# Kernel optimization log

Hardware: AMD Instinct MI355X
Metric: run time of the kernel (lower is better)

The kernel has to match this reference:

```python
import jax, jax.numpy as jnp
import numpy as np

B, L = 2048, 64          # batch, seq_len (title length)
H, DK = 20, 20           # heads, per-head dim (d_k = d_v = 20)
V, D = 50000, 300        # vocab, word embedding dim
HD = H * DK              # 400


def setup_inputs() -> dict:
    key = jax.random.key(0)
    ks = jax.random.split(key, 12)
    n = lambda k, shape, sc: jax.random.normal(k, shape, dtype=jnp.float32) * sc
    return {
        "text": jax.random.randint(ks[0], (B, L), 0, V),
        "emb": n(ks[1], (V, D), 0.1),
        "WQ": n(ks[2], (D, HD), 0.05), "bQ": jnp.zeros((HD,), jnp.float32),
        "WK": n(ks[3], (D, HD), 0.05), "bK": jnp.zeros((HD,), jnp.float32),
        "WV": n(ks[4], (D, HD), 0.05), "bV": jnp.zeros((HD,), jnp.float32),
        "W1": n(ks[5], (HD, 200), 0.05), "b1": jnp.zeros((200,), jnp.float32),
        "W2": n(ks[6], (200, 1), 0.05), "b2": jnp.zeros((1,), jnp.float32),
    }


def reference(text, emb, WQ, bQ, WK, bK, WV, bV, W1, b1, W2, b2):
    # Embedding lookup (dropout is identity at eval)
    x = emb[text]                                            # [B, L, D]
    b, l = x.shape[0], x.shape[1]

    # Multi-head self-attention with unstable exp-softmax (faithful to source)
    q = (x @ WQ + bQ).reshape(b, l, H, DK)                   # [B, L, H, DK]
    k = (x @ WK + bK).reshape(b, l, H, DK)
    v = (x @ WV + bV).reshape(b, l, H, DK)
    scores = jnp.einsum("bqhd,bkhd->bhqk", q, k) / np.float32(np.sqrt(DK))
    scores = jnp.exp(scores)                                 # [B, H, L, L]
    attn = scores / (jnp.sum(scores, axis=-1, keepdims=True) + 1e-8)
    ctx = jnp.einsum("bhqk,bkhd->bqhd", attn, v).reshape(b, l, HD)  # [B, L, 400]

    # Additive attention pooling (linear -> tanh -> linear -> exp-normalize -> weighted sum)
    e = jnp.tanh(ctx @ W1 + b1)                              # [B, L, 200]
    alpha = jnp.exp(e @ W2 + b2)                             # [B, L, 1]
    alpha = alpha / (jnp.sum(alpha, axis=1, keepdims=True) + 1e-8)
    return jnp.sum(ctx * alpha, axis=1)                      # [B, 400]
```

## Files before the change

kernel.cpp:

```cpp
#include <hip/hip_runtime.h>
#include <hip/hip_bf16.h>

#define B_   2048
#define L_   64
#define H_   20
#define DK_  20
#define D_   300
#define HD_  400
#define F1_  200

typedef __attribute__((ext_vector_type(8))) short short8;
typedef __attribute__((ext_vector_type(4))) float f32x4;

#define WQKV_TILES   800
#define W1_TILES     169
#define W1_OFF_U16   409600
#define CTX_OFF_B    1048576
#define CTX_BYTES    (2048L * 64 * 400 * 2)
#define WS_FULL      (CTX_OFF_B + CTX_BYTES)

__device__ __forceinline__ float b2f(unsigned short u) {
    union { unsigned int i; float f; } v; v.i = ((unsigned int)u) << 16; return v.f;
}
__device__ __forceinline__ unsigned int f2b2(float a, float b) {
    union { __hip_bfloat162 h; unsigned int u; } cv;
    cv.h = __float22bfloat162_rn(make_float2(a, b));
    return cv.u;
}
__device__ __forceinline__ unsigned short f2b(float a) {
    union { __hip_bfloat16 h; unsigned short u; } cv;
    cv.h = __float2bfloat16(a);
    return cv.u;
}
__device__ __forceinline__ float rcpf(float x) { return __builtin_amdgcn_rcpf(x); }
__device__ __forceinline__ float rlane(float v, int l) {
    return __int_as_float(__builtin_amdgcn_readlane(__float_as_int(v), l));
}

__global__ void pack_weights_new(const float* __restrict__ WQ, const float* __restrict__ WK,
                                 const float* __restrict__ WV, const float* __restrict__ W1,
                                 unsigned short* __restrict__ wsp)
{
    const int tid  = blockIdx.x * 256 + threadIdx.x;
    const int frag = tid >> 6, l = tid & 63;
    if (frag >= WQKV_TILES + W1_TILES) return;
    const int octet = l >> 4, lo = l & 15;
    unsigned short v[8];
    if (frag < WQKV_TILES) {
        const int hg = frag / 80, r = frag % 80, kt = r / 8, nt = r % 8;
        const int nl = nt * 16 + lo;
        const int sel = (nl < 120) ? nl / 40 : 0;
        const int within = nl % 40;
        const int h2 = within / 20, d = within % 20;
        const int col = (hg * 2 + h2) * 20 + d;
        const float* W = (sel == 0) ? WQ : (sel == 1) ? WK : WV;
        #pragma unroll
        for (int j = 0; j < 8; ++j) {
            const int k = kt * 32 + octet * 8 + j;
            const float f = (nl < 120 && k < 300) ? W[k * 400 + col] : 0.f;
            v[j] = f2b(f);
        }
    } else {
        const int f2 = frag - WQKV_TILES, kt = f2 / 13, nt = f2 % 13;
        const int n = nt * 16 + lo;
        #pragma unroll
        for (int j = 0; j < 8; ++j) {
            const int k = kt * 32 + octet * 8 + j;
            const float f = (n < 200 && k < 400) ? W1[k * 200 + n] : 0.f;
            v[j] = f2b(f);
        }
    }
    unsigned short* dst = wsp + (long)frag * 512 + l * 8;
    *(ushort4*)(dst)     = make_ushort4(v[0], v[1], v[2], v[3]);
    *(ushort4*)(dst + 4) = make_ushort4(v[4], v[5], v[6], v[7]);
}

template<int S>
__device__ __forceinline__ void a_step(int hg0, int w, int l, bool act, int selbase,
                                       const unsigned short* xp,
                                       const unsigned short* __restrict__ wsp,
                                       const float* bq, f32x4 slab[][4])
{
    #pragma unroll
    for (int s = 0; s < S; ++s) {
        const float bv = act ? bq[selbase + (hg0 + s) * 40] : 0.f;
        #pragma unroll
        for (int mt = 0; mt < 4; ++mt) slab[s][mt] = (f32x4){bv, bv, bv, bv};
    }
    for (int kt = 0; kt < 10; ++kt) {
        short8 a[4];
        #pragma unroll
        for (int mt = 0; mt < 4; ++mt)
            a[mt] = *(const short8*)(xp + ((mt * 10 + kt) * 64 + l) * 8);
        #pragma unroll
        for (int s = 0; s < S; ++s) {
            const short8 bf = *(const short8*)(wsp + ((long)((hg0 + s) * 80 + kt * 8 + w) * 512) + l * 8);
            #pragma unroll
            for (int mt = 0; mt < 4; ++mt)
                slab[s][mt] = __builtin_amdgcn_mfma_f32_16x16x32_bf16(a[mt], bf, slab[s][mt], 0, 0, 0);
        }
    }
}

__device__ __forceinline__ void attn_hg_body(
    int hg, const f32x4* sl, int b, int t, int l, int w,
    bool act, int sel, int baseQK, int baseV, int quad,
    unsigned short* trans, unsigned short* vBs, unsigned short* stage,
    float* rsum_s, unsigned short* __restrict__ ctx_ws)
{
    if (hg > 0) {
        for (int u = t; u < 640; u += 512) {
            const int row = u / 10, c4 = u - row * 10;
            const ushort4 v = *(const ushort4*)(stage + row * 40 + c4 * 4);
            *(ushort4*)(ctx_ws + ((long)(b * 64 + row)) * 400 + (hg - 1) * 40 + c4 * 4) = v;
        }
    }
    if (act) {
        const unsigned int u01a = f2b2(sl[0][0], sl[0][1]), u23a = f2b2(sl[0][2], sl[0][3]);
        const unsigned int u01b = f2b2(sl[1][0], sl[1][1]), u23b = f2b2(sl[1][2], sl[1][3]);
        const unsigned int u01c = f2b2(sl[2][0], sl[2][1]), u23c = f2b2(sl[2][2], sl[2][3]);
        const unsigned int u01d = f2b2(sl[3][0], sl[3][1]), u23d = f2b2(sl[3][2], sl[3][3]);
        const unsigned int p01[4] = {u01a, u01b, u01c, u01d};
        const unsigned int p23[4] = {u23a, u23b, u23c, u23d};
        if (sel < 2) {
            #pragma unroll
            for (int mt = 0; mt < 4; ++mt) {
                const int a0 = baseQK + mt * 512;
                trans[a0]      = (unsigned short)p01[mt];
                trans[a0 + 8]  = (unsigned short)(p01[mt] >> 16);
                trans[a0 + 16] = (unsigned short)p23[mt];
                trans[a0 + 24] = (unsigned short)(p23[mt] >> 16);
            }
        } else {
            #pragma unroll
            for (int mt = 0; mt < 4; ++mt) {
                const int bm = baseV + (mt >> 1) * 1024 + (mt & 1) * 256;
                #pragma unroll
                for (int ii = 0; ii < 4; ++ii) {
                    const int tq = quad * 4 + ii;
                    const unsigned int uu = (ii < 2) ? p01[mt] : p23[mt];
                    vBs[bm + (tq >> 3) * 128 + (tq & 7)] =
                        (unsigned short)((ii & 1) ? (uu >> 16) : uu);
                }
            }
        }
    }
    __syncthreads();

    const int h = w >> 2, jt = w & 3;
    f32x4 accS[4];
    #pragma unroll
    for (int mt = 0; mt < 4; ++mt) accS[mt] = (f32x4){0.f, 0.f, 0.f, 0.f};
    {
        short8 qa[4];
        #pragma unroll
        for (int mt = 0; mt < 4; ++mt)
            qa[mt] = *(const short8*)(trans + ((h * 4 + mt) * 64 + l) * 8);
        const short8 kb = *(const short8*)(trans + 4096 + ((h * 4 + jt) * 64 + l) * 8);
        #pragma unroll
        for (int mt = 0; mt < 4; ++mt)
            accS[mt] = __builtin_amdgcn_mfma_f32_16x16x32_bf16(qa[mt], kb, accS[mt], 0, 0, 0);
    }
    __syncthreads();
    {
        const int jtok = jt * 16 + (l & 15);
        const int ktp = jtok >> 5;
        #pragma unroll
        for (int mt = 0; mt < 4; ++mt) {
            const float e0 = __expf(accS[mt][0] * 0.22360679774997896f);
            const float e1 = __expf(accS[mt][1] * 0.22360679774997896f);
            const float e2 = __expf(accS[mt][2] * 0.22360679774997896f);
            const float e3 = __expf(accS[mt][3] * 0.22360679774997896f);
            const unsigned int u01 = f2b2(e0, e1), u23 = f2b2(e2, e3);
            const int a0 = (((h * 4 + mt) * 2 + ktp) * 64 + quad * 4 + ((jtok & 31) >> 3) * 16) * 8 + (jtok & 7);
            trans[a0]      = (unsigned short)u01;
            trans[a0 + 8]  = (unsigned short)(u01 >> 16);
            trans[a0 + 16] = (unsigned short)u23;
            trans[a0 + 24] = (unsigned short)(u23 >> 16);
        }
    }
    __syncthreads();

    const int dnt = (w >> 1) & 1, mh = w & 1;
    f32x4 accC[2];
    accC[0] = (f32x4){0.f, 0.f, 0.f, 0.f};
    accC[1] = (f32x4){0.f, 0.f, 0.f, 0.f};
    #pragma unroll
    for (int ktc = 0; ktc < 2; ++ktc) {
        const short8 vb = *(const short8*)(vBs + (((h * 2 + ktc) * 2 + dnt) * 64 + l) * 8);
        #pragma unroll
        for (int mi = 0; mi < 2; ++mi) {
            const int mt = mh * 2 + mi;
            const short8 pa = *(const short8*)(trans + (((h * 4 + mt) * 2 + ktc) * 64 + l) * 8);
            accC[mi] = __builtin_amdgcn_mfma_f32_16x16x32_bf16(pa, vb, accC[mi], 0, 0, 0);
        }
    }
    if (dnt == 1 && (l & 15) == 4) {
        #pragma unroll
        for (int mi = 0; mi < 2; ++mi)
            #pragma unroll
            for (int ii = 0; ii < 4; ++ii)
                rsum_s[h * 64 + (mh * 2 + mi) * 16 + quad * 4 + ii] = accC[mi][ii];
    }
    __syncthreads();
    if (hg < 9) {
        unsigned int* tz = (unsigned int*)trans;
        for (int i = t; i < 4096; i += 512) tz[i] = 0u;
    }
    {
        const int dloc = dnt * 16 + (l & 15);
        if (dloc < 20) {
            const int cl = h * 20 + dloc;
            #pragma unroll
            for (int mi = 0; mi < 2; ++mi) {
                const int mt = mh * 2 + mi;
                float vv[4];
                #pragma unroll
                for (int ii = 0; ii < 4; ++ii) {
                    const int tok = mt * 16 + quad * 4 + ii;
                    vv[ii] = accC[mi][ii] * rcpf(rsum_s[h * 64 + tok] + 1e-8f);
                }
                const unsigned int u01 = f2b2(vv[0], vv[1]), u23 = f2b2(vv[2], vv[3]);
                const int base = (mt * 16 + quad * 4) * 40 + cl;
                stage[base]       = (unsigned short)u01;
                stage[base + 40]  = (unsigned short)(u01 >> 16);
                stage[base + 80]  = (unsigned short)u23;
                stage[base + 120] = (unsigned short)(u23 >> 16);
            }
        }
    }
    __syncthreads();
}

__global__ __launch_bounds__(512, 4)
void te_attn(const int* __restrict__ text,
             const float* __restrict__ emb,
             const float* __restrict__ bQ, const float* __restrict__ bK,
             const float* __restrict__ bV,
             const unsigned short* __restrict__ wsp,
             unsigned short* __restrict__ ctx_ws)
{
    __shared__ unsigned short x_pack[4 * 10 * 64 * 8];
    __shared__ unsigned short trans[8192];
    __shared__ unsigned short vB[4096];
    __shared__ unsigned short ctx_stage[64 * 40];
    __shared__ float bqkv_s[1200];
    __shared__ float rsum_s[128];
    __shared__ int   text_s[64];

    const int b = blockIdx.x;
    const int t = threadIdx.x;
    const int l = t & 63;
    const int w = t >> 6;
    const int quad = l >> 4;

    {
        unsigned int* xz = (unsigned int*)x_pack;
        for (int i = t; i < 10240; i += 512) xz[i] = 0u;
        unsigned int* tz = (unsigned int*)trans;
        for (int i = t; i < 4096; i += 512) tz[i] = 0u;
        unsigned int* vz = (unsigned int*)vB;
        for (int i = t; i < 2048; i += 512) {
            const int tile = i >> 8;
            const int lane_v = (i & 255) >> 2;
            vz[i] = ((tile & 1) == 1 && (lane_v & 15) == 4) ? 0x3F803F80u : 0u;
        }
        for (int i = t; i < 1200; i += 512)
            bqkv_s[i] = (i < 400) ? bQ[i] : (i < 800) ? bK[i - 400] : bV[i - 800];
        if (t < 64) text_s[t] = text[b * L_ + t];
    }
    __syncthreads();

    for (int u = t; u < 64 * 75; u += 512) {
        const int r = u / 75, c4 = u - r * 75, k = c4 * 4;
        const float4 f = *(const float4*)(emb + (long)text_s[r] * D_ + k);
        const int mt = r >> 4, kt = k >> 5;
        const int ld = (r & 15) + ((k & 31) >> 3) * 16;
        const unsigned int u01 = f2b2(f.x, f.y), u23 = f2b2(f.z, f.w);
        *(uint2*)(x_pack + ((mt * 10 + kt) * 64 + ld) * 8 + (k & 7)) = make_uint2(u01, u23);
    }
    __syncthreads();

    const int nl = w * 16 + (l & 15);
    const bool act = nl < 120;
    int sel = 0, h2 = 0, d = 0;
    if (act) { sel = nl / 40; const int within = nl % 40; h2 = within / 20; d = within % 20; }
    const int baseQK = h2 * 2048 + (quad * 4 + (d >> 3) * 16) * 8 + (d & 7) + ((sel == 1) ? 4096 : 0);
    const int baseV  = h2 * 2048 + (d >> 4) * 512 + (d & 15) * 8;
    const int selbase = sel * 400 + h2 * 20 + d;

    f32x4 slab[4][4];
    a_step<4>(0, w, l, act, selbase, x_pack, wsp, bqkv_s, slab);
    attn_hg_body(0, slab[0], b, t, l, w, act, sel, baseQK, baseV, quad, trans, vB, ctx_stage, rsum_s, ctx_ws);
    attn_hg_body(1, slab[1], b, t, l, w, act, sel, baseQK, baseV, quad, trans, vB, ctx_stage, rsum_s, ctx_ws);
    attn_hg_body(2, slab[2], b, t, l, w, act, sel, baseQK, baseV, quad, trans, vB, ctx_stage, rsum_s, ctx_ws);
    attn_hg_body(3, slab[3], b, t, l, w, act, sel, baseQK, baseV, quad, trans, vB, ctx_stage, rsum_s, ctx_ws);
    a_step<3>(4, w, l, act, selbase, x_pack, wsp, bqkv_s, slab);
    attn_hg_body(4, slab[0], b, t, l, w, act, sel, baseQK, baseV, quad, trans, vB, ctx_stage, rsum_s, ctx_ws);
    attn_hg_body(5, slab[1], b, t, l, w, act, sel, baseQK, baseV, quad, trans, vB, ctx_stage, rsum_s, ctx_ws);
    attn_hg_body(6, slab[2], b, t, l, w, act, sel, baseQK, baseV, quad, trans, vB, ctx_stage, rsum_s, ctx_ws);
    a_step<3>(7, w, l, act, selbase, x_pack, wsp, bqkv_s, slab);
    attn_hg_body(7, slab[0], b, t, l, w, act, sel, baseQK, baseV, quad, trans, vB, ctx_stage, rsum_s, ctx_ws);
    attn_hg_body(8, slab[1], b, t, l, w, act, sel, baseQK, baseV, quad, trans, vB, ctx_stage, rsum_s, ctx_ws);
    attn_hg_body(9, slab[2], b, t, l, w, act, sel, baseQK, baseV, quad, trans, vB, ctx_stage, rsum_s, ctx_ws);

    for (int u = t; u < 640; u += 512) {
        const int row = u / 10, c4 = u - row * 10;
        const ushort4 v = *(const ushort4*)(ctx_stage + row * 40 + c4 * 4);
        *(ushort4*)(ctx_ws + ((long)(b * 64 + row)) * 400 + 9 * 40 + c4 * 4) = v;
    }
}

__global__ __launch_bounds__(512, 4)
void te_pool(const unsigned short* __restrict__ ctx_ws,
             const float* __restrict__ b1, const float* __restrict__ W2,
             const float* __restrict__ b2,
             const unsigned short* __restrict__ wsp,
             float* __restrict__ out)
{
    __shared__ unsigned short ctxA[4 * 13 * 64 * 8];
    __shared__ float b1_s[208], w2_s[208];
    __shared__ float aacc_s[64], alpha_s[64];
    __shared__ float inv_asum_s;

    const int b = blockIdx.x;
    const int t = threadIdx.x;
    const int l = t & 63;
    const int w = t >> 6;

    {
        unsigned int* cz = (unsigned int*)ctxA;
        for (int i = t; i < 1024; i += 512) {
            const int mt = i >> 8;
            cz[(mt * 13 + 12) * 256 + (i & 255)] = 0u;
        }
        if (t < 208) { b1_s[t] = (t < 200) ? b1[t] : 0.f; w2_s[t] = (t < 200) ? W2[t] : 0.f; }
        if (t >= 208 && t < 272) aacc_s[t - 208] = 0.f;
    }
    __syncthreads();

    for (int u = t; u < 3200; u += 512) {
        const int row = u / 50, c8 = u - row * 50;
        const int col = c8 * 8;
        const short8 v = *(const short8*)(ctx_ws + ((long)(b * 64 + row)) * 400 + col);
        const int mt = row >> 4, ktx = col >> 5;
        *(short8*)(ctxA + ((mt * 13 + ktx) * 64 + (row & 15) + ((col & 31) >> 3) * 16) * 8) = v;
    }
    __syncthreads();

    {
        f32x4 accD[2][4];
        #pragma unroll
        for (int g = 0; g < 2; ++g)
            #pragma unroll
            for (int mt = 0; mt < 4; ++mt) accD[g][mt] = (f32x4){0.f, 0.f, 0.f, 0.f};
        const int nta = w, ntb = w + 8;
        for (int kt = 0; kt < 13; ++kt) {
            short8 ca[4];
            #pragma unroll
            for (int mt = 0; mt < 4; ++mt)
                ca[mt] = *(const short8*)(ctxA + ((mt * 13 + kt) * 64 + l) * 8);
            const short8 wb0 = *(const short8*)(wsp + W1_OFF_U16 + ((long)(kt * 13 + nta) * 512) + l * 8);
            #pragma unroll
            for (int mt = 0; mt < 4; ++mt)
                accD[0][mt] = __builtin_amdgcn_mfma_f32_16x16x32_bf16(ca[mt], wb0, accD[0][mt], 0, 0, 0);
            if (ntb < 13) {
                const short8 wb1 = *(const short8*)(wsp + W1_OFF_U16 + ((long)(kt * 13 + ntb) * 512) + l * 8);
                #pragma unroll
                for (int mt = 0; mt < 4; ++mt)
                    accD[1][mt] = __builtin_amdgcn_mfma_f32_16x16x32_bf16(ca[mt], wb1, accD[1][mt], 0, 0, 0);
            }
        }
        float part[4][4];
        #pragma unroll
        for (int mt = 0; mt < 4; ++mt)
            #pragma unroll
            for (int ii = 0; ii < 4; ++ii) part[mt][ii] = 0.f;
        #pragma unroll
        for (int g = 0; g < 2; ++g) {
            const int ntv = (g == 0) ? nta : ntb;
            if (ntv < 13) {
                const int colb = ntv * 16 + (l & 15);
                const float b1v = b1_s[colb], w2v = w2_s[colb];
                #pragma unroll
                for (int mt = 0; mt < 4; ++mt)
                    #pragma unroll
                    for (int ii = 0; ii < 4; ++ii) {
                        const float x = accD[g][mt][ii] + b1v;
                        const float ex = __expf(2.f * x);
                        const float th = 1.f - 2.f * rcpf(ex + 1.f);
                        part[mt][ii] += th * w2v;
                    }
            }
        }
        #pragma unroll
        for (int mt = 0; mt < 4; ++mt)
            #pragma unroll
            for (int ii = 0; ii < 4; ++ii) {
                float v = part[mt][ii];
                v += __shfl_xor(v, 1, 64); v += __shfl_xor(v, 2, 64);
                v += __shfl_xor(v, 4, 64); v += __shfl_xor(v, 8, 64);
                if ((l & 15) == 0)
                    atomicAdd(&aacc_s[mt * 16 + (l >> 4) * 4 + ii], v);
            }
    }
    __syncthreads();

    if (t < 64) {
        const float a = __expf(aacc_s[t] + b2[0]);
        alpha_s[t] = a;
        float s = a;
        s += __shfl_xor(s, 32, 64); s += __shfl_xor(s, 16, 64);
        s += __shfl_xor(s, 8, 64);  s += __shfl_xor(s, 4, 64);
        s += __shfl_xor(s, 2, 64);  s += __shfl_xor(s, 1, 64);
        if (t == 0) inv_asum_s = 1.f / (s + 1e-8f);
    }
    __syncthreads();

    if (t < HD_) {
        const int c = t;
        const int ktx = c >> 5, ldo = ((c & 31) >> 3) * 16, el = c & 7;
        float a = 0.f;
        for (int tok = 0; tok < 64; ++tok) {
            const unsigned short us =
                ctxA[(((tok >> 4) * 13 + ktx) * 64 + (tok & 15) + ldo) * 8 + el];
            a = fmaf(b2f(us), alpha_s[tok], a);
        }
        out[(long)b * HD_ + c] = a * inv_asum_s;
    }
}

#define XS   324
#define CS   404
#define QS   21
#define SS   66

__global__ __launch_bounds__(512, 2)
void te_fused_fb(const int* __restrict__ text, const float* __restrict__ emb,
                 const float* __restrict__ WQ, const float* __restrict__ bQ,
                 const float* __restrict__ WK, const float* __restrict__ bK,
                 const float* __restrict__ WV, const float* __restrict__ bV,
                 const float* __restrict__ W1, const float* __restrict__ b1,
                 const float* __restrict__ W2, const float* __restrict__ b2,
                 float* __restrict__ out)
{
    __shared__ int            text_s[L_];
    __shared__ unsigned short x_s[L_ * XS];
    __shared__ unsigned short ctx_s[L_ * CS];
    __shared__ float          qkv_s[3 * 2 * L_ * QS];
    __shared__ unsigned short sc_s[2 * L_ * SS];
    __shared__ float          aacc_s[L_], alpha_s[L_];
    __shared__ float          inv_asum_s;

    const int b = blockIdx.x, t = threadIdx.x, lane = t & 63, wv = t >> 6;
    if (t < 64) text_s[t] = text[b * L_ + t];
    if (t >= 64 && t < 128) aacc_s[t - 64] = 0.f;
    __syncthreads();
    for (int u = t; u < L_ * 75; u += 512) {
        int l = u / 75, c4 = u - l * 75;
        const float4 f = *(const float4*)(emb + (long)text_s[l] * D_ + c4 * 4);
        ushort4 o; o.x = f2b(f.x); o.y = f2b(f.y); o.z = f2b(f.z); o.w = f2b(f.w);
        *(ushort4*)(x_s + l * XS + c4 * 4) = o;
    }
    __syncthreads();
    for (int hp = 0; hp < H_ / 2; ++hp) {
        const int h0 = hp * 2;
        if (t < 480) {
            const int rt = t & 15, ct = t >> 4, r0 = rt * 4, qc = ct * 4;
            const int sel = qc / 40, rem = qc - sel * 40, hh = rem / 20, cc = rem - hh * 20;
            const float* W = (sel == 0) ? WQ : (sel == 1) ? WK : WV;
            const float* bias = (sel == 0) ? bQ : (sel == 1) ? bK : bV;
            const int col0 = (h0 + hh) * 20 + cc;
            float acc[4][4];
            #pragma unroll
            for (int j = 0; j < 4; ++j) {
                const float bj = bias[col0 + j];
                acc[0][j] = bj; acc[1][j] = bj; acc[2][j] = bj; acc[3][j] = bj;
            }
            const float* Wp = W + col0;
            for (int c4 = 0; c4 < 75; ++c4) {
                const int d0 = c4 * 4;
                float xv[4][4]; float4 wvv[4];
                #pragma unroll
                for (int i = 0; i < 4; ++i) {
                    ushort4 xu = *(const ushort4*)(x_s + (r0 + i) * XS + d0);
                    xv[i][0] = b2f(xu.x); xv[i][1] = b2f(xu.y);
                    xv[i][2] = b2f(xu.z); xv[i][3] = b2f(xu.w);
                }
                #pragma unroll
                for (int dd = 0; dd < 4; ++dd)
                    wvv[dd] = *(const float4*)(Wp + (long)(d0 + dd) * HD_);
                #pragma unroll
                for (int dd = 0; dd < 4; ++dd)
                    #pragma unroll
                    for (int i = 0; i < 4; ++i) {
                        acc[i][0] = fmaf(xv[i][dd], wvv[dd].x, acc[i][0]);
                        acc[i][1] = fmaf(xv[i][dd], wvv[dd].y, acc[i][1]);
                        acc[i][2] = fmaf(xv[i][dd], wvv[dd].z, acc[i][2]);
                        acc[i][3] = fmaf(xv[i][dd], wvv[dd].w, acc[i][3]);
                    }
            }
            #pragma unroll
            for (int i = 0; i < 4; ++i)
                #pragma unroll
                for (int j = 0; j < 4; ++j)
                    qkv_s[((sel * 2 + hh) * L_ + r0 + i) * QS + cc + j] = acc[i][j];
        }
        __syncthreads();
        {
            const int j = lane, ig = wv & 3, hh = wv >> 2;
            float qreg[20], kreg[20];
            const float* qrow = &qkv_s[((0 * 2 + hh) * L_ + j) * QS];
            const float* krow = &qkv_s[((1 * 2 + hh) * L_ + j) * QS];
            #pragma unroll
            for (int dd = 0; dd < 20; ++dd) { qreg[dd] = qrow[dd]; kreg[dd] = krow[dd]; }
            for (int ii = 0; ii < 16; ++ii) {
                const int i = ig * 16 + ii;
                float s = 0.f;
                #pragma unroll
                for (int dd = 0; dd < 20; ++dd) s = fmaf(rlane(qreg[dd], i), kreg[dd], s);
                sc_s[(hh * L_ + i) * SS + j] = f2b(__expf(s * 0.22360679774997896f));
            }
        }
        __syncthreads();
        {
            const int i = lane, dg = wv, head = dg >> 2, dv0 = (dg & 3) * 5;
            float vreg[5];
            #pragma unroll
            for (int m = 0; m < 5; ++m)
                vreg[m] = qkv_s[((2 * 2 + head) * L_ + i) * QS + dv0 + m];
            float acc[5] = {0.f, 0.f, 0.f, 0.f, 0.f};
            float rsum = 0.f;
            const unsigned short* prow = &sc_s[(head * L_ + i) * SS];
            for (int jj = 0; jj < 64; ++jj) {
                const float p = b2f(prow[jj]);
                rsum += p;
                #pragma unroll
                for (int m = 0; m < 5; ++m) acc[m] = fmaf(p, rlane(vreg[m], jj), acc[m]);
            }
            const float inv = 1.f / (rsum + 1e-8f);
            const int col0 = (h0 + head) * 20 + dv0;
            #pragma unroll
            for (int m = 0; m < 5; ++m) ctx_s[i * CS + col0 + m] = f2b(acc[m] * inv);
        }
        __syncthreads();
    }
    for (int tau = t; tau < 800; tau += 512) {
        const int rt = tau & 15, cm = tau >> 4, r0 = rt * 4, m0 = cm * 4;
        float acc[4][4];
        #pragma unroll
        for (int j = 0; j < 4; ++j) {
            const float bj = b1[m0 + j];
            acc[0][j] = bj; acc[1][j] = bj; acc[2][j] = bj; acc[3][j] = bj;
        }
        for (int c4 = 0; c4 < 100; ++c4) {
            const int c0 = c4 * 4;
            float cv[4][4]; float4 wv1[4];
            #pragma unroll
            for (int i = 0; i < 4; ++i) {
                ushort4 cu = *(const ushort4*)(ctx_s + (r0 + i) * CS + c0);
                cv[i][0] = b2f(cu.x); cv[i][1] = b2f(cu.y);
                cv[i][2] = b2f(cu.z); cv[i][3] = b2f(cu.w);
            }
            #pragma unroll
            for (int dd = 0; dd < 4; ++dd)
                wv1[dd] = *(const float4*)(W1 + (long)(c0 + dd) * F1_ + m0);
            #pragma unroll
            for (int dd = 0; dd < 4; ++dd)
                #pragma unroll
                for (int i = 0; i < 4; ++i) {
                    acc[i][0] = fmaf(cv[i][dd], wv1[dd].x, acc[i][0]);
                    acc[i][1] = fmaf(cv[i][dd], wv1[dd].y, acc[i][1]);
                    acc[i][2] = fmaf(cv[i][dd], wv1[dd].z, acc[i][2]);
                    acc[i][3] = fmaf(cv[i][dd], wv1[dd].w, acc[i][3]);
                }
        }
        float w2l[4];
        #pragma unroll
        for (int j = 0; j < 4; ++j) w2l[j] = W2[m0 + j];
        #pragma unroll
        for (int i = 0; i < 4; ++i) {
            float ap = 0.f;
            #pragma unroll
            for (int j = 0; j < 4; ++j) ap += tanhf(acc[i][j]) * w2l[j];
            atomicAdd(&aacc_s[r0 + i], ap);
        }
    }
    __syncthreads();
    if (t < 64) {
        const float a = __expf(aacc_s[t] + b2[0]);
        alpha_s[t] = a;
        float s = a;
        s += __shfl_xor(s, 32, 64); s += __shfl_xor(s, 16, 64);
        s += __shfl_xor(s, 8, 64);  s += __shfl_xor(s, 4, 64);
        s += __shfl_xor(s, 2, 64);  s += __shfl_xor(s, 1, 64);
        if (t == 0) inv_asum_s = 1.f / (s + 1e-8f);
    }
    __syncthreads();
    if (t < HD_) {
        float a = 0.f;
        for (int l2 = 0; l2 < 64; ++l2)
            a = fmaf(b2f(ctx_s[l2 * CS + t]), alpha_s[l2], a);
        out[(long)b * HD_ + t] = a * inv_asum_s;
    }
}

extern "C" void kernel_launch(void* const* d_in, const int* in_sizes, int n_in,
                              void* d_out, int out_size, void* d_ws, size_t ws_size,
                              hipStream_t stream) {
    const int*   text = (const int*)d_in[0];
    const float* emb  = (const float*)d_in[1];
    const float* WQ   = (const float*)d_in[2];
    const float* bQ   = (const float*)d_in[3];
    const float* WK   = (const float*)d_in[4];
    const float* bK   = (const float*)d_in[5];
    const float* WV   = (const float*)d_in[6];
    const float* bV   = (const float*)d_in[7];
    const float* W1   = (const float*)d_in[8];
    const float* b1   = (const float*)d_in[9];
    const float* W2   = (const float*)d_in[10];
    const float* b2   = (const float*)d_in[11];
    float*       out  = (float*)d_out;

    if (ws_size >= (size_t)WS_FULL) {
        unsigned short* wsp    = (unsigned short*)d_ws;
        unsigned short* ctx_ws = (unsigned short*)((char*)d_ws + CTX_OFF_B);
        const int total_frag_threads = (WQKV_TILES + W1_TILES) * 64;
        pack_weights_new<<<(total_frag_threads + 255) / 256, 256, 0, stream>>>(WQ, WK, WV, W1, wsp);
        te_attn<<<B_, 512, 0, stream>>>(text, emb, bQ, bK, bV, wsp, ctx_ws);
        te_pool<<<B_, 512, 0, stream>>>(ctx_ws, b1, W2, b2, wsp, out);
    } else {
        te_fused_fb<<<B_, 512, 0, stream>>>(text, emb, WQ, bQ, WK, bK, WV, bV,
                                            W1, b1, W2, b2, out);
    }
}
```

Baseline: 347.6 us.

## Fuse W1 projection and tanh scoring into attention kernel per head group

The ctx@W1 GEMM and the tanh/W2 scoring are moved out of the pooling kernel and into the attention kernel. Each finished head group's staged context slice is multiplied by a repacked per-head-group W1 fragment, so the pooling kernel no longer has to reload and re-layout the whole context for an MFMA pass. Per-token logits go through the output buffer, and a slimmer output kernel does the softmax and the weighted sum. The QKV slab batching also drops from 4/3/3 to 3/3/2/2 head groups to free registers for the new accumulators. In exchange, the attention kernel gains register pressure and extra global weight loads per head group, and it stores temporary logits in the output array.

New measurement: 540.7 us. +55.6%, slower.

```diff
diff --git a/kernel.cpp b/kernel.cpp
--- a/kernel.cpp
+++ b/kernel.cpp
@@ -13,8 +13,8 @@
 typedef __attribute__((ext_vector_type(4))) float f32x4;
 
 #define WQKV_TILES   800
-#define W1_TILES     169
-#define W1_OFF_U16   409600
+#define W1C_OFF_U16  409600
+#define W1_KT0_FR    130
 #define CTX_OFF_B    1048576
 #define CTX_BYTES    (2048L * 64 * 400 * 2)
 #define WS_FULL      (CTX_OFF_B + CTX_BYTES)
@@ -37,15 +37,14 @@
     return __int_as_float(__builtin_amdgcn_readlane(__float_as_int(v), l));
 }
 
-__global__ void pack_weights_new(const float* __restrict__ WQ, const float* __restrict__ WK,
-                                 const float* __restrict__ WV, const float* __restrict__ W1,
-                                 unsigned short* __restrict__ wsp)
+__global__ void pack_weights_v2(const float* __restrict__ WQ, const float* __restrict__ WK,
+                                const float* __restrict__ WV, const float* __restrict__ W1,
+                                unsigned short* __restrict__ wsp)
 {
     const int tid  = blockIdx.x * 256 + threadIdx.x;
     const int frag = tid >> 6, l = tid & 63;
-    if (frag >= WQKV_TILES + W1_TILES) return;
+    if (frag >= 1060) return;
     const int octet = l >> 4, lo = l & 15;
-    unsigned short v[8];
     if (frag < WQKV_TILES) {
         const int hg = frag / 80, r = frag % 80, kt = r / 8, nt = r % 8;
         const int nl = nt * 16 + lo;
@@ -54,25 +53,44 @@
         const int h2 = within / 20, d = within % 20;
         const int col = (hg * 2 + h2) * 20 + d;
         const float* W = (sel == 0) ? WQ : (sel == 1) ? WK : WV;
+        unsigned short v[8];
         #pragma unroll
         for (int j = 0; j < 8; ++j) {
             const int k = kt * 32 + octet * 8 + j;
             const float f = (nl < 120 && k < 300) ? W[k * 400 + col] : 0.f;
             v[j] = f2b(f);
         }
+        unsigned short* dst = wsp + (long)frag * 512 + l * 8;
+        *(ushort4*)(dst)     = make_ushort4(v[0], v[1], v[2], v[3]);
+        *(ushort4*)(dst + 4) = make_ushort4(v[4], v[5], v[6], v[7]);
+    } else if (frag < 800 + W1_KT0_FR) {
+        const int f2 = frag - 800, hg = f2 / 13, nt = f2 % 13;
+        const int n = nt * 16 + lo;
+        unsigned short v[8];
+        #pragma unroll
+        for (int j = 0; j < 8; ++j) {
+            const int kl = octet * 8 + j;
+            const float f = (n < 200) ? W1[(hg * 40 + kl) * 200 + n] : 0.f;
+            v[j] = f2b(f);
+        }
+        unsigned short* dst = wsp + W1C_OFF_U16 + (long)(hg * 13 + nt) * 640 + l * 8;
+        *(ushort4*)(dst)     = make_ushort4(v[0], v[1], v[2], v[3]);
+        *(ushort4*)(dst + 4) = make_ushort4(v[4], v[5], v[6], v[7]);
     } else {
-        const int f2 = frag - WQKV_TILES, kt = f2 / 13, nt = f2 % 13;
-        const int n = nt * 16 + lo;
-        #pragma unroll
-        for (int j = 0; j < 8; ++j) {
-            const int k = kt * 32 + octet * 8 + j;
-            const float f = (n < 200 && k < 400) ? W1[k * 200 + n] : 0.f;
-            v[j] = f2b(f);
-        }
-    }
-    unsigned short* dst = wsp + (long)frag * 512 + l * 8;
-    *(ushort4*)(dst)     = make_ushort4(v[0], v[1], v[2], v[3]);
-    *(ushort4*)(dst + 4) = make_ushort4(v[4], v[5], v[6], v[7]);
+        const int f2 = frag - 800 - W1_KT0_FR, hg = f2 / 13, nt = f2 % 13;
+        if (l < 16) {
+            const int n = nt * 16 + l;
+            unsigned short v[8];
+            #pragma unroll
+            for (int j = 0; j < 8; ++j) {
+                const float f = (n < 200) ? W1[(hg * 40 + 32 + j) * 200 + n] : 0.f;
+                v[j] = f2b(f);
+            }
+            unsigned short* dst = wsp + W1C_OFF_U16 + (long)(hg * 13 + nt) * 640 + 512 + l * 8;
+            *(ushort4*)(dst)     = make_ushort4(v[0], v[1], v[2], v[3]);
+            *(ushort4*)(dst + 4) = make_ushort4(v[4], v[5], v[6], v[7]);
+        }
+    }
 }
 
 template<int S>
@@ -102,11 +120,48 @@
     }
 }
 
+__device__ __forceinline__ void d_accum(int hg, int l, int w, int quad,
+                                        const unsigned short* stage,
+                                        const unsigned short* __restrict__ wsp,
+                                        f32x4 accD[2][4])
+{
+    short8 a0[4], a1[4];
+    const short8 zz = {0, 0, 0, 0, 0, 0, 0, 0};
+    #pragma unroll
+    for (int mt = 0; mt < 4; ++mt) {
+        const int tok = mt * 16 + (l & 15);
+        a0[mt] = *(const short8*)(stage + tok * 40 + quad * 8);
+        a1[mt] = (quad == 0) ? *(const short8*)(stage + tok * 40 + 32) : zz;
+    }
+    const int nta = w, ntb = w + 8;
+    {
+        const unsigned short* base = wsp + W1C_OFF_U16 + (long)(hg * 13 + nta) * 640;
+        const short8 wb0 = *(const short8*)(base + l * 8);
+        const short8 wb1 = *(const short8*)(base + 512 + (l & 15) * 8);
+        #pragma unroll
+        for (int mt = 0; mt < 4; ++mt) {
+            accD[0][mt] = __builtin_amdgcn_mfma_f32_16x16x32_bf16(a0[mt], wb0, accD[0][mt], 0, 0, 0);
+            accD[0][mt] = __builtin_amdgcn_mfma_f32_16x16x32_bf16(a1[mt], wb1, accD[0][mt], 0, 0, 0);
+        }
+    }
+    if (ntb < 13) {
+        const unsigned short* base = wsp + W1C_OFF_U16 + (long)(hg * 13 + ntb) * 640;
+        const short8 wb0 = *(const short8*)(base + l * 8);
+        const short8 wb1 = *(const short8*)(base + 512 + (l & 15) * 8);
+        #pragma unroll
+        for (int mt = 0; mt < 4; ++mt) {
+            accD[1][mt] = __builtin_amdgcn_mfma_f32_16x16x32_bf16(a0[mt], wb0, accD[1][mt], 0, 0, 0);
+            accD[1][mt] = __builtin_amdgcn_mfma_f32_16x16x32_bf16(a1[mt], wb1, accD[1][mt], 0, 0, 0);
+        }
+    }
+}
+
 __device__ __forceinline__ void attn_hg_body(
     int hg, const f32x4* sl, int b, int t, int l, int w,
     bool act, int sel, int baseQK, int baseV, int quad,
     unsigned short* trans, unsigned short* vBs, unsigned short* stage,
-    float* rsum_s, unsigned short* __restrict__ ctx_ws)
+    float* rsum_s, unsigned short* __restrict__ ctx_ws,
+    const unsigned short* __restrict__ wsp, f32x4 accD[2][4])
 {
     if (hg > 0) {
         for (int u = t; u < 640; u += 512) {
@@ -114,6 +169,7 @@
             const ushort4 v = *(const ushort4*)(stage + row * 40 + c4 * 4);
             *(ushort4*)(ctx_ws + ((long)(b * 64 + row)) * 400 + (hg - 1) * 40 + c4 * 4) = v;
         }
+        d_accum(hg - 1, l, w, quad, stage, wsp, accD);
     }
     if (act) {
         const unsigned int u01a = f2b2(sl[0][0], sl[0][1]), u23a = f2b2(sl[0][2], sl[0][3]);
@@ -237,15 +293,19 @@
              const float* __restrict__ emb,
              const float* __restrict__ bQ, const float* __restrict__ bK,
              const float* __restrict__ bV,
+             const float* __restrict__ b1, const float* __restrict__ W2,
              const unsigned short* __restrict__ wsp,
-             unsigned short* __restrict__ ctx_ws)
+             unsigned short* __restrict__ ctx_ws,
+             float* __restrict__ logit_out)
 {
     __shared__ unsigned short x_pack[4 * 10 * 64 * 8];
     __shared__ unsigned short trans[8192];
     __shared__ unsigned short vB[4096];
     __shared__ unsigned short ctx_stage[64 * 40];
     __shared__ float bqkv_s[1200];
+    __shared__ float b1_s[208], w2_s[208];
     __shared__ float rsum_s[128];
+    __shared__ float aacc_s[64];
     __shared__ int   text_s[64];
 
     const int b = blockIdx.x;
@@ -267,7 +327,9 @@
         }
         for (int i = t; i < 1200; i += 512)
             bqkv_s[i] = (i < 400) ? bQ[i] : (i < 800) ? bK[i - 400] : bV[i - 800];
-        if (t < 64) text_s[t] = text[b * L_ + t];
+        if (t < 208) { b1_s[t] = (t < 200) ? b1[t] : 0.f; w2_s[t] = (t < 200) ? W2[t] : 0.f; }
+        if (t >= 208 && t < 272) aacc_s[t - 208] = 0.f;
+        if (t >= 272 && t < 336) text_s[t - 272] = text[b * L_ + (t - 272)];
     }
     __syncthreads();
 
@@ -289,144 +351,100 @@
     const int baseV  = h2 * 2048 + (d >> 4) * 512 + (d & 15) * 8;
     const int selbase = sel * 400 + h2 * 20 + d;
 
-    f32x4 slab[4][4];
-    a_step<4>(0, w, l, act, selbase, x_pack, wsp, bqkv_s, slab);
-    attn_hg_body(0, slab[0], b, t, l, w, act, sel, baseQK, baseV, quad, trans, vB, ctx_stage, rsum_s, ctx_ws);
-    attn_hg_body(1, slab[1], b, t, l, w, act, sel, baseQK, baseV, quad, trans, vB, ctx_stage, rsum_s, ctx_ws);
-    attn_hg_body(2, slab[2], b, t, l, w, act, sel, baseQK, baseV, quad, trans, vB, ctx_stage, rsum_s, ctx_ws);
-    attn_hg_body(3, slab[3], b, t, l, w, act, sel, baseQK, baseV, quad, trans, vB, ctx_stage, rsum_s, ctx_ws);
-    a_step<3>(4, w, l, act, selbase, x_pack, wsp, bqkv_s, slab);
-    attn_hg_body(4, slab[0], b, t, l, w, act, sel, baseQK, baseV, quad, trans, vB, ctx_stage, rsum_s, ctx_ws);
-    attn_hg_body(5, slab[1], b, t, l, w, act, sel, baseQK, baseV, quad, trans, vB, ctx_stage, rsum_s, ctx_ws);
-    attn_hg_body(6, slab[2], b, t, l, w, act, sel, baseQK, baseV, quad, trans, vB, ctx_stage, rsum_s, ctx_ws);
-    a_step<3>(7, w, l, act, selbase, x_pack, wsp, bqkv_s, slab);
-    attn_hg_body(7, slab[0], b, t, l, w, act, sel, baseQK, baseV, quad, trans, vB, ctx_stage, rsum_s, ctx_ws);
-    attn_hg_body(8, slab[1], b, t, l, w, act, sel, baseQK, baseV, quad, trans, vB, ctx_stage, rsum_s, ctx_ws);
-    attn_hg_body(9, slab[2], b, t, l, w, act, sel, baseQK, baseV, quad, trans, vB, ctx_stage, rsum_s, ctx_ws);
+    f32x4 accD[2][4];
+    #pragma unroll
+    for (int g = 0; g < 2; ++g)
+        #pragma unroll
+        for (int mt = 0; mt < 4; ++mt) accD[g][mt] = (f32x4){0.f, 0.f, 0.f, 0.f};
+
+    f32x4 slab[3][4];
+    a_step<3>(0, w, l, act, selbase, x_pack, wsp, bqkv_s, slab);
+    attn_hg_body(0, slab[0], b, t, l, w, act, sel, baseQK, baseV, quad, trans, vB, ctx_stage, rsum_s, ctx_ws, wsp, accD);
+    attn_hg_body(1, slab[1], b, t, l, w, act, sel, baseQK, baseV, quad, trans, vB, ctx_stage, rsum_s, ctx_ws, wsp, accD);
+    attn_hg_body(2, slab[2], b, t, l, w, act, sel, baseQK, baseV, quad, trans, vB, ctx_stage, rsum_s, ctx_ws, wsp, accD);
+    a_step<3>(3, w, l, act, selbase, x_pack, wsp, bqkv_s, slab);
+    attn_hg_body(3, slab[0], b, t, l, w, act, sel, baseQK, baseV, quad, trans, vB, ctx_stage, rsum_s, ctx_ws, wsp, accD);
+    attn_hg_body(4, slab[1], b, t, l, w, act, sel, baseQK, baseV, quad, trans, vB, ctx_stage, rsum_s, ctx_ws, wsp, accD);
+    attn_hg_body(5, slab[2], b, t, l, w, act, sel, baseQK, baseV, quad, trans, vB, ctx_stage, rsum_s, ctx_ws, wsp, accD);
+    a_step<2>(6, w, l, act, selbase, x_pack, wsp, bqkv_s, slab);
+    attn_hg_body(6, slab[0], b, t, l, w, act, sel, baseQK, baseV, quad, trans, vB, ctx_stage, rsum_s, ctx_ws, wsp, accD);
+    attn_hg_body(7, slab[1], b, t, l, w, act, sel, baseQK, baseV, quad, trans, vB, ctx_stage, rsum_s, ctx_ws, wsp, accD);
+    a_step<2>(8, w, l, act, selbase, x_pack, wsp, bqkv_s, slab);
+    attn_hg_body(8, slab[0], b, t, l, w, act, sel, baseQK, baseV, quad, trans, vB, ctx_stage, rsum_s, ctx_ws, wsp, accD);
+    attn_hg_body(9, slab[1], b, t, l, w, act, sel, baseQK, baseV, quad, trans, vB, ctx_stage, rsum_s, ctx_ws, wsp, accD);
 
     for (int u = t; u < 640; u += 512) {
         const int row = u / 10, c4 = u - row * 10;
         const ushort4 v = *(const ushort4*)(ctx_stage + row * 40 + c4 * 4);
         *(ushort4*)(ctx_ws + ((long)(b * 64 + row)) * 400 + 9 * 40 + c4 * 4) = v;
     }
+    d_accum(9, l, w, quad, ctx_stage, wsp, accD);
+
+    #pragma unroll
+    for (int g = 0; g < 2; ++g) {
+        const int ntv = (g == 0) ? w : w + 8;
+        if (ntv < 13) {
+            const int colb = ntv * 16 + (l & 15);
+            const float b1v = b1_s[colb], w2v = w2_s[colb];
+            #pragma unroll
+            for (int mt = 0; mt < 4; ++mt) {
+                float part[4];
+                #pragma unroll
+                for (int ii = 0; ii < 4; ++ii) {
+                    const float x = accD[g][mt][ii] + b1v;
+                    const float ex = __expf(2.f * x);
+                    part[ii] = (1.f - 2.f * rcpf(ex + 1.f)) * w2v;
+                }
+                #pragma unroll
+                for (int ii = 0; ii < 4; ++ii) {
+                    float v = part[ii];
+                    v += __shfl_xor(v, 1, 64); v += __shfl_xor(v, 2, 64);
+                    v += __shfl_xor(v, 4, 64); v += __shfl_xor(v, 8, 64);
+                    if ((l & 15) == 0)
+                        atomicAdd(&aacc_s[mt * 16 + quad * 4 + ii], v);
+                }
+            }
+        }
+    }
+    __syncthreads();
+    if (t < 64)
+        logit_out[(long)b * HD_ + t] = aacc_s[t];
 }
 
 __global__ __launch_bounds__(512, 4)
-void te_pool(const unsigned short* __restrict__ ctx_ws,
-             const float* __restrict__ b1, const float* __restrict__ W2,
-             const float* __restrict__ b2,
-             const unsigned short* __restrict__ wsp,
-             float* __restrict__ out)
+void te_out(const unsigned short* __restrict__ ctx_ws,
+            const float* __restrict__ b2,
+            float* __restrict__ out)
 {
-    __shared__ unsigned short ctxA[4 * 13 * 64 * 8];
-    __shared__ float b1_s[208], w2_s[208];
-    __shared__ float aacc_s[64], alpha_s[64];
-    __shared__ float inv_asum_s;
+    __shared__ unsigned short ctx_l[64 * 400];
+    __shared__ float alpha_s[64];
 
     const int b = blockIdx.x;
     const int t = threadIdx.x;
-    const int l = t & 63;
-    const int w = t >> 6;
-
-    {
-        unsigned int* cz = (unsigned int*)ctxA;
-        for (int i = t; i < 1024; i += 512) {
-            const int mt = i >> 8;
-            cz[(mt * 13 + 12) * 256 + (i & 255)] = 0u;
-        }
-        if (t < 208) { b1_s[t] = (t < 200) ? b1[t] : 0.f; w2_s[t] = (t < 200) ? W2[t] : 0.f; }
-        if (t >= 208 && t < 272) aacc_s[t - 208] = 0.f;
-    }
-    __syncthreads();
+
+    float av = 0.f;
+    if (t < 64) av = __expf(out[(long)b * HD_ + t] + b2[0]);
 
     for (int u = t; u < 3200; u += 512) {
         const int row = u / 50, c8 = u - row * 50;
-        const int col = c8 * 8;
-        const short8 v = *(const short8*)(ctx_ws + ((long)(b * 64 + row)) * 400 + col);
-        const int mt = row >> 4, ktx = col >> 5;
-        *(short8*)(ctxA + ((mt * 13 + ktx) * 64 + (row & 15) + ((col & 31) >> 3) * 16) * 8) = v;
-    }
-    __syncthreads();
-
-    {
-        f32x4 accD[2][4];
-        #pragma unroll
-        for (int g = 0; g < 2; ++g)
-            #pragma unroll
-            for (int mt = 0; mt < 4; ++mt) accD[g][mt] = (f32x4){0.f, 0.f, 0.f, 0.f};
-        const int nta = w, ntb = w + 8;
-        for (int kt = 0; kt < 13; ++kt) {
-            short8 ca[4];
-            #pragma unroll
-            for (int mt = 0; mt < 4; ++mt)
-                ca[mt] = *(const short8*)(ctxA + ((mt * 13 + kt) * 64 + l) * 8);
-            const short8 wb0 = *(const short8*)(wsp + W1_OFF_U16 + ((long)(kt * 13 + nta) * 512) + l * 8);
-            #pragma unroll
-            for (int mt = 0; mt < 4; ++mt)
-                accD[0][mt] = __builtin_amdgcn_mfma_f32_16x16x32_bf16(ca[mt], wb0, accD[0][mt], 0, 0, 0);
-            if (ntb < 13) {
-                const short8 wb1 = *(const short8*)(wsp + W1_OFF_U16 + ((long)(kt * 13 + ntb) * 512) + l * 8);
-                #pragma unroll
-                for (int mt = 0; mt < 4; ++mt)
-                    accD[1][mt] = __builtin_amdgcn_mfma_f32_16x16x32_bf16(ca[mt], wb1, accD[1][mt], 0, 0, 0);
-            }
-        }
-        float part[4][4];
-        #pragma unroll
-        for (int mt = 0; mt < 4; ++mt)
-            #pragma unroll
-            for (int ii = 0; ii < 4; ++ii) part[mt][ii] = 0.f;
-        #pragma unroll
-        for (int g = 0; g < 2; ++g) {
-            const int ntv = (g == 0) ? nta : ntb;
-            if (ntv < 13) {
-                const int colb = ntv * 16 + (l & 15);
-                const float b1v = b1_s[colb], w2v = w2_s[colb];
-                #pragma unroll
-                for (int mt = 0; mt < 4; ++mt)
-                    #pragma unroll
-                    for (int ii = 0; ii < 4; ++ii) {
-                        const float x = accD[g][mt][ii] + b1v;
-                        const float ex = __expf(2.f * x);
-                        const float th = 1.f - 2.f * rcpf(ex + 1.f);
-                        part[mt][ii] += th * w2v;
-                    }
-            }
-        }
-        #pragma unroll
-        for (int mt = 0; mt < 4; ++mt)
-            #pragma unroll
-            for (int ii = 0; ii < 4; ++ii) {
-                float v = part[mt][ii];
-                v += __shfl_xor(v, 1, 64); v += __shfl_xor(v, 2, 64);
-                v += __shfl_xor(v, 4, 64); v += __shfl_xor(v, 8, 64);
-                if ((l & 15) == 0)
-                    atomicAdd(&aacc_s[mt * 16 + (l >> 4) * 4 + ii], v);
-            }
-    }
-    __syncthreads();
-
+        *(short8*)(ctx_l + row * 400 + c8 * 8) =
+            *(const short8*)(ctx_ws + ((long)(b * 64 + row)) * 400 + c8 * 8);
+    }
     if (t < 64) {
-        const float a = __expf(aacc_s[t] + b2[0]);
-        alpha_s[t] = a;
-        float s = a;
+        float s = av;
         s += __shfl_xor(s, 32, 64); s += __shfl_xor(s, 16, 64);
         s += __shfl_xor(s, 8, 64);  s += __shfl_xor(s, 4, 64);
         s += __shfl_xor(s, 2, 64);  s += __shfl_xor(s, 1, 64);
-        if (t == 0) inv_asum_s = 1.f / (s + 1e-8f);
+        alpha_s[t] = av * rcpf(s + 1e-8f);
     }
     __syncthreads();
 
     if (t < HD_) {
-        const int c = t;
-        const int ktx = c >> 5, ldo = ((c & 31) >> 3) * 16, el = c & 7;
         float a = 0.f;
-        for (int tok = 0; tok < 64; ++tok) {
-            const unsigned short us =
-                ctxA[(((tok >> 4) * 13 + ktx) * 64 + (tok & 15) + ldo) * 8 + el];
-            a = fmaf(b2f(us), alpha_s[tok], a);
-        }
-        out[(long)b * HD_ + c] = a * inv_asum_s;
+        #pragma unroll 4
+        for (int tok = 0; tok < 64; ++tok)
+            a = fmaf(b2f(ctx_l[tok * 400 + t]), alpha_s[tok], a);
+        out[(long)b * HD_ + t] = a;
     }
 }
 
@@ -625,10 +643,9 @@
     if (ws_size >= (size_t)WS_FULL) {
         unsigned short* wsp    = (unsigned short*)d_ws;
         unsigned short* ctx_ws = (unsigned short*)((char*)d_ws + CTX_OFF_B);
-        const int total_frag_threads = (WQKV_TILES + W1_TILES) * 64;
-        pack_weights_new<<<(total_frag_threads + 255) / 256, 256, 0, stream>>>(WQ, WK, WV, W1, wsp);
-        te_attn<<<B_, 512, 0, stream>>>(text, emb, bQ, bK, bV, wsp, ctx_ws);
-        te_pool<<<B_, 512, 0, stream>>>(ctx_ws, b1, W2, b2, wsp, out);
+        pack_weights_v2<<<(1060 * 64 + 255) / 256, 256, 0, stream>>>(WQ, WK, WV, W1, wsp);
+        te_attn<<<B_, 512, 0, stream>>>(text, emb, bQ, bK, bV, b1, W2, wsp, ctx_ws, out);
+        te_out<<<B_, 512, 0, stream>>>(ctx_ws, b2, out);
     } else {
         te_fused_fb<<<B_, 512, 0, stream>>>(text, emb, WQ, bQ, WK, bK, WV, bV,
                                             W1, b1, W2, b2, out);
```
